# Kernel tuning notes

Hardware: AMD Instinct MI355X
Metric: run time of the kernel (lower is better)

Reference implementation:

```python
import jax, jax.numpy as jnp
import numpy as np
from jax import lax

BASE = 10000.0
N_STATE = 4096
N_HEAD = 32
H_DIM = N_STATE // N_HEAD          # 128
NUM_ROT = H_DIM // 2               # 64
BATCH, SEQ = 4, 2048


def setup_inputs() -> dict:
    key = jax.random.key(0)
    k1, k2, k3, k4 = jax.random.split(key, 4)
    x = jax.random.normal(k1, (BATCH, SEQ, N_STATE), dtype=jnp.float32)
    thetas = jax.random.normal(k2, (NUM_ROT,), dtype=jnp.float32) * 0.1
    rotation_pairs = jax.random.uniform(k3, (NUM_ROT, 2), dtype=jnp.float32) * H_DIM
    theta_scale = jnp.ones((1,), dtype=jnp.float32)
    rotation_matrix = jnp.eye(H_DIM, dtype=jnp.float32) + 0.02 * jax.random.normal(k4, (H_DIM, H_DIM), dtype=jnp.float32)
    inv_freq = (1.0 / BASE ** (jnp.arange(0, H_DIM, 2, dtype=jnp.float32) / H_DIM)).astype(jnp.float32)
    return {"x": x, "thetas": thetas, "rotation_pairs": rotation_pairs,
            "theta_scale": theta_scale, "rotation_matrix": rotation_matrix,
            "inv_freq": inv_freq, "n_head": N_HEAD}


def _apply(x, thetas, rotation_pairs, theta_scale, rotation_matrix, inv_freq, n_head):
    B, S, n_state = x.shape
    h_dim = rotation_matrix.shape[0]
    xf = x.reshape(B, S, n_head, h_dim).reshape(-1, h_dim)  # [B*S*H, h_dim]

    idx = rotation_pairs.astype(jnp.int32)          # [R,2] Givens pair indices
    th = thetas * theta_scale[0]                    # [R]

    def body(xc, inp):
        i, j, t = inp
        c, s = jnp.cos(t), jnp.sin(t)
        xi = xc[:, i]
        xj = xc[:, j]
        same = (i == j)
        # x @ G touches only columns i and j (matches torch G construction,
        # including the i==j overwrite case where G[i,i] ends as cos)
        vi = jnp.where(same, xi * c, xi * c + xj * s)
        vj = jnp.where(same, xi * c, -xi * s + xj * c)
        xc = xc.at[:, i].set(vi)
        xc = xc.at[:, j].set(vj)
        return xc, None

    xf, _ = lax.scan(body, xf, (idx[:, 0], idx[:, 1], th))
    xf = xf @ rotation_matrix                       # learned h_dim x h_dim mix
    xh = xf.reshape(B, S, n_head, h_dim)

    pos = jnp.arange(S, dtype=jnp.float32)
    sinusoid = pos[:, None] * inv_freq[None, :]     # [S, h_dim/2]
    sin = jnp.sin(sinusoid)[None, :, None, :]
    cos = jnp.cos(sinusoid)[None, :, None, :]
    x1 = xh[..., ::2]
    x2 = xh[..., 1::2]
    out = jnp.concatenate([x1 * cos - x2 * sin, x1 * sin + x2 * cos], axis=-1)
    return out.reshape(B, S, n_state)


def reference(x, thetas, rotation_pairs, theta_scale, rotation_matrix, inv_freq, n_head):
    return _apply(x, thetas, rotation_pairs, theta_scale, rotation_matrix, inv_freq, n_head)
```

## Files before the change

kernel.cpp:

```cpp
#include <hip/hip_runtime.h>
#include <hip/hip_bf16.h>
#include <math.h>

#define SEQ_LEN 2048
#define NROWS (4 * 2048 * 32)
#define NSTRIPS (NROWS / 16)

typedef short bf16x8 __attribute__((ext_vector_type(8)));
typedef float f32x4 __attribute__((ext_vector_type(4)));

__device__ __forceinline__ unsigned short f2bf(float f) {
    union { float f; unsigned int i; } v; v.f = f;
    unsigned int r = v.i + 0x7FFFu + ((v.i >> 16) & 1u);
    return (unsigned short)(r >> 16);
}

__global__ void prep_kernel(const float* __restrict__ thetas,
                            const float* __restrict__ pairs,
                            const float* __restrict__ tscale,
                            const float* __restrict__ rotmat,
                            unsigned short* __restrict__ Bsw) {
    __shared__ float M[128][128];
    __shared__ float Cv[64], Sv[64];
    __shared__ int   Iv[64], Jv[64];
    const int t = threadIdx.x;
    if (t < 64) {
        const float th = thetas[t] * tscale[0];
        Cv[t] = cosf(th);
        Sv[t] = sinf(th);
        int i = (int)pairs[2 * t];
        int j = (int)pairs[2 * t + 1];
        Iv[t] = min(max(i, 0), 127);
        Jv[t] = min(max(j, 0), 127);
    }
    for (int d = 0; d < 128; ++d) M[d][t] = rotmat[d * 128 + t];
    __syncthreads();
    for (int r = 63; r >= 0; --r) {
        const int i = Iv[r], j = Jv[r];
        const float c = Cv[r], s = Sv[r];
        if (i == j) {
            M[i][t] *= c;
        } else {
            const float a = M[i][t], b = M[j][t];
            M[i][t] = c * a - s * b;
            M[j][t] = s * a + c * b;
        }
    }
    __syncthreads();
    for (int idx = t; idx < 32 * 64; idx += 128) {
        const int f = idx >> 6, lane = idx & 63;
        const int kk = f >> 3, nt = f & 7;
        const int krow = kk * 32 + (lane >> 4) * 8;
        const int m = lane & 15;
        const int col = (nt < 4) ? (8 * m + 2 * nt) : (8 * m + 2 * (nt - 4) + 1);
        unsigned short* dst = Bsw + (size_t)idx * 8;
#pragma unroll
        for (int j2 = 0; j2 < 8; ++j2) dst[j2] = f2bf(M[krow + j2][col]);
    }
}

__global__ __launch_bounds__(256, 4) void rope_kernel(
        const float* __restrict__ x,
        const unsigned short* __restrict__ Bsw,
        const float* __restrict__ invfreq,
        float* __restrict__ out) {
    __shared__ f32x4 Blds[2048];
    {
        const f32x4* src = (const f32x4*)Bsw;
#pragma unroll
        for (int i = 0; i < 8; ++i)
            Blds[threadIdx.x + 256 * i] = src[threadIdx.x + 256 * i];
    }
    __syncthreads();

    const int lane = threadIdx.x & 63;
    const int wave = (int)(blockIdx.x * (blockDim.x >> 6) + (threadIdx.x >> 6));
    const int nwaves = (int)(gridDim.x * (blockDim.x >> 6));
    const int m = lane & 15;
    const int quad = lane >> 4;
    const bf16x8* Bf = (const bf16x8*)Blds;

    const float invf = invfreq[lane];

    for (int strip = wave; strip < NSTRIPS; strip += nwaves) {
        const int r0 = strip * 16;
        const float* xrow = x + (size_t)(r0 + m) * 128 + quad * 8;
        f32x4 lo[4], hi[4];
#pragma unroll
        for (int kk = 0; kk < 4; ++kk) {
            lo[kk] = *(const f32x4*)(xrow + kk * 32);
            hi[kk] = *(const f32x4*)(xrow + kk * 32 + 4);
        }

        const int s_pos = (r0 >> 5) & (SEQ_LEN - 1);
        float sn_l, cs_l;
        sincosf((float)s_pos * invf, &sn_l, &cs_l);

        bf16x8 A[4];
#pragma unroll
        for (int kk = 0; kk < 4; ++kk) {
            union { __hip_bfloat162 h; unsigned int u; } c0, c1, c2, c3;
            c0.h = __float22bfloat162_rn(make_float2(lo[kk][0], lo[kk][1]));
            c1.h = __float22bfloat162_rn(make_float2(lo[kk][2], lo[kk][3]));
            c2.h = __float22bfloat162_rn(make_float2(hi[kk][0], hi[kk][1]));
            c3.h = __float22bfloat162_rn(make_float2(hi[kk][2], hi[kk][3]));
            union { unsigned int u[4]; bf16x8 v; } a;
            a.u[0] = c0.u; a.u[1] = c1.u; a.u[2] = c2.u; a.u[3] = c3.u;
            A[kk] = a.v;
        }

        f32x4 acc[8];
#pragma unroll
        for (int nt = 0; nt < 8; ++nt) acc[nt] = (f32x4){0.f, 0.f, 0.f, 0.f};

#pragma unroll
        for (int kk = 0; kk < 4; ++kk)
#pragma unroll
            for (int nt = 0; nt < 8; ++nt)
                acc[nt] = __builtin_amdgcn_mfma_f32_16x16x32_bf16(
                    A[kk], Bf[(kk * 8 + nt) * 64 + lane], acc[nt], 0, 0, 0);

        float cs[4], sn[4];
#pragma unroll
        for (int nt = 0; nt < 4; ++nt) {
            cs[nt] = __shfl(cs_l, 4 * m + nt, 64);
            sn[nt] = __shfl(sn_l, 4 * m + nt, 64);
        }
        float* orow = out + (size_t)(r0 + quad * 4) * 128;
#pragma unroll
        for (int rr = 0; rr < 4; ++rr) {
            f32x4 ve, vo;
#pragma unroll
            for (int nt = 0; nt < 4; ++nt) {
                const float ye = acc[nt][rr];
                const float yo = acc[nt + 4][rr];
                ve[nt] = ye * cs[nt] - yo * sn[nt];
                vo[nt] = ye * sn[nt] + yo * cs[nt];
            }
            *(f32x4*)(orow + (size_t)rr * 128 + 4 * m)      = ve;
            *(f32x4*)(orow + (size_t)rr * 128 + 64 + 4 * m) = vo;
        }
    }
}

extern "C" void kernel_launch(void* const* d_in, const int* in_sizes, int n_in,
                              void* d_out, int out_size, void* d_ws, size_t ws_size,
                              hipStream_t stream) {
    const float* x      = (const float*)d_in[0];
    const float* thetas = (const float*)d_in[1];
    const float* pairs  = (const float*)d_in[2];
    const float* tscale = (const float*)d_in[3];
    const float* rotmat = (const float*)d_in[4];
    const float* invfr  = (const float*)d_in[5];
    float* out = (float*)d_out;
    unsigned short* Bsw = (unsigned short*)d_ws;

    prep_kernel<<<1, 128, 0, stream>>>(thetas, pairs, tscale, rotmat, Bsw);
    rope_kernel<<<2048, 256, 0, stream>>>(x, Bsw, invfr, out);
}
```

Measured before the change: 299.8 us.

## Prefetch both x strips before the LDS barrier and load B via global_load_lds

The rope kernel now issues the global loads for both of its fixed strips, plus their sincos, before the barrier that waits for the B-matrix LDS fill, so input latency overlaps the LDS setup. The B fill uses direct global-to-LDS loads instead of going through registers. The grid-stride loop is replaced by exactly two strips per wave, hardcoded to the 2048-block grid. The prep kernel is widened to 256 threads for a coalesced matrix load. Register pressure rises from holding two strips' inputs at once.

```diff
diff --git a/kernel.cpp b/kernel.cpp
--- a/kernel.cpp
+++ b/kernel.cpp
@@ -33,21 +33,25 @@
         Iv[t] = min(max(i, 0), 127);
         Jv[t] = min(max(j, 0), 127);
     }
-    for (int d = 0; d < 128; ++d) M[d][t] = rotmat[d * 128 + t];
+    float* Mf = &M[0][0];
+#pragma unroll 8
+    for (int idx = t; idx < 128 * 128; idx += 256) Mf[idx] = rotmat[idx];
     __syncthreads();
-    for (int r = 63; r >= 0; --r) {
-        const int i = Iv[r], j = Jv[r];
-        const float c = Cv[r], s = Sv[r];
-        if (i == j) {
-            M[i][t] *= c;
-        } else {
-            const float a = M[i][t], b = M[j][t];
-            M[i][t] = c * a - s * b;
-            M[j][t] = s * a + c * b;
+    if (t < 128) {
+        for (int r = 63; r >= 0; --r) {
+            const int i = Iv[r], j = Jv[r];
+            const float c = Cv[r], s = Sv[r];
+            if (i == j) {
+                M[i][t] *= c;
+            } else {
+                const float a = M[i][t], b = M[j][t];
+                M[i][t] = c * a - s * b;
+                M[j][t] = s * a + c * b;
+            }
         }
     }
     __syncthreads();
-    for (int idx = t; idx < 32 * 64; idx += 128) {
+    for (int idx = t; idx < 32 * 64; idx += 256) {
         const int f = idx >> 6, lane = idx & 63;
         const int kk = f >> 3, nt = f & 7;
         const int krow = kk * 32 + (lane >> 4) * 8;
@@ -65,36 +69,58 @@
         const float* __restrict__ invfreq,
         float* __restrict__ out) {
     __shared__ f32x4 Blds[2048];
+    const int tid = threadIdx.x;
+    const int lane = tid & 63;
+    const int w = tid >> 6;
     {
-        const f32x4* src = (const f32x4*)Bsw;
+        const char* gbase = (const char*)Bsw;
 #pragma unroll
-        for (int i = 0; i < 8; ++i)
-            Blds[threadIdx.x + 256 * i] = src[threadIdx.x + 256 * i];
+        for (int i = 0; i < 8; ++i) {
+            const int fi = i * 256 + w * 64;
+            __builtin_amdgcn_global_load_lds(
+                (const __attribute__((address_space(1))) unsigned int*)
+                    (gbase + (size_t)(fi + lane) * 16),
+                (__attribute__((address_space(3))) unsigned int*)&Blds[fi],
+                16, 0, 0);
+        }
     }
+
+    const int wave = (int)(blockIdx.x * 4 + w);
+    const int m = lane & 15;
+    const int quad = lane >> 4;
+    const int sA = wave;
+    const int sB = wave + 8192;
+
+    const float* xA = x + (size_t)(sA * 16 + m) * 128 + quad * 8;
+    const float* xB = x + (size_t)(sB * 16 + m) * 128 + quad * 8;
+    f32x4 loA[4], hiA[4], loB[4], hiB[4];
+#pragma unroll
+    for (int kk = 0; kk < 4; ++kk) {
+        loA[kk] = *(const f32x4*)(xA + kk * 32);
+        hiA[kk] = *(const f32x4*)(xA + kk * 32 + 4);
+    }
+#pragma unroll
+    for (int kk = 0; kk < 4; ++kk) {
+        loB[kk] = *(const f32x4*)(xB + kk * 32);
+        hiB[kk] = *(const f32x4*)(xB + kk * 32 + 4);
+    }
+
+    const float invf = invfreq[lane];
+    float snA, csA, snB, csB;
+    sincosf((float)((sA * 16 >> 5) & (SEQ_LEN - 1)) * invf, &snA, &csA);
+    sincosf((float)((sB * 16 >> 5) & (SEQ_LEN - 1)) * invf, &snB, &csB);
+
     __syncthreads();
 
-    const int lane = threadIdx.x & 63;
-    const int wave = (int)(blockIdx.x * (blockDim.x >> 6) + (threadIdx.x >> 6));
-    const int nwaves = (int)(gridDim.x * (blockDim.x >> 6));
-    const int m = lane & 15;
-    const int quad = lane >> 4;
     const bf16x8* Bf = (const bf16x8*)Blds;
 
-    const float invf = invfreq[lane];
-
-    for (int strip = wave; strip < NSTRIPS; strip += nwaves) {
-        const int r0 = strip * 16;
-        const float* xrow = x + (size_t)(r0 + m) * 128 + quad * 8;
-        f32x4 lo[4], hi[4];
 #pragma unroll
-        for (int kk = 0; kk < 4; ++kk) {
-            lo[kk] = *(const f32x4*)(xrow + kk * 32);
-            hi[kk] = *(const f32x4*)(xrow + kk * 32 + 4);
-        }
-
-        const int s_pos = (r0 >> 5) & (SEQ_LEN - 1);
-        float sn_l, cs_l;
-        sincosf((float)s_pos * invf, &sn_l, &cs_l);
+    for (int half = 0; half < 2; ++half) {
+        const int r0 = (half ? sB : sA) * 16;
+        const f32x4* lo = half ? loB : loA;
+        const f32x4* hi = half ? hiB : hiA;
+        const float sn_l = half ? snB : snA;
+        const float cs_l = half ? csB : csA;
 
         bf16x8 A[4];
 #pragma unroll
@@ -155,6 +181,6 @@
     float* out = (float*)d_out;
     unsigned short* Bsw = (unsigned short*)d_ws;
 
-    prep_kernel<<<1, 128, 0, stream>>>(thetas, pairs, tscale, rotmat, Bsw);
+    prep_kernel<<<1, 256, 0, stream>>>(thetas, pairs, tscale, rotmat, Bsw);
     rope_kernel<<<2048, 256, 0, stream>>>(x, Bsw, invfr, out);
 }
```

After: 263.0 us. -12.3%, faster.
